# Kernel optimization log

Hardware: AMD Instinct MI355X
Metric: run time of the kernel (lower is better)

The kernel has to match this reference:

```python
import jax, jax.numpy as jnp
import numpy as np

OUT_SIZE = 14
CUTOFF = 0.2
VAR0 = 4            # var[0], mixin_factor = 0.0 -> current std = var[0]
BETA = 4.0
N_SQ = OUT_SIZE * OUT_SIZE
TAU = 0.5 / N_SQ
BATCH = 256
CHANNELS = 512


def _gkern_np(kernlen, std, vmin, vmax):
    n = np.arange(kernlen) - (kernlen - 1) / 2.0
    w = np.exp(-(n ** 2) / (2.0 * std * std))
    g = np.outer(w, w)
    return g * (vmax - vmin) + vmin


def _build_templates():
    n = OUT_SIZE
    base = _gkern_np(2 * n - 1, VAR0, -CUTOFF, 1.0)
    base = np.maximum(base, 0.0) * 2.0 - 1.0
    base = TAU * np.clip(BETA * base / n, -1.0, None)  # clamp(min=-1) only
    # unfold(0,n,1).unfold(1,n,1).reshape(-1,n,n) == sliding windows, row-major
    t = np.lib.stride_tricks.sliding_window_view(base, (n, n)).reshape(-1, n, n)
    t = np.flip(t, axis=0).copy()  # torch.flip(templates, dims=(0,))
    templates_f = jnp.asarray(t, jnp.float32)                    # (n^2, n, n)
    neg = -TAU * jnp.ones((1, n, n), jnp.float32)
    templates_b = jnp.concatenate([templates_f, neg], axis=0)    # (n^2+1, n, n)
    alpha = N_SQ / (1.0 + N_SQ)
    p_T = jnp.asarray(
        np.array([alpha / N_SQ] * N_SQ + [1.0 - alpha], np.float32))  # (n^2+1,)
    return templates_f, templates_b, p_T


def setup_inputs() -> dict:
    key = jax.random.key(0)
    templates_f, templates_b, p_T = _build_templates()
    x = jax.random.normal(key, (BATCH, CHANNELS, OUT_SIZE, OUT_SIZE), jnp.float32)
    return {"x": x, "templates_f": templates_f,
            "templates_b": templates_b, "p_T": p_T}


def reference(x, templates_f, templates_b, p_T):
    B, C, H, W = x.shape
    tau = 0.5 / (H * W)
    # max_pool2d with kernel == full spatial extent -> flat argmax per (b, c)
    idx = jnp.argmax(x.reshape(B, C, H * W), axis=-1)            # (B, C) int
    sel = templates_f[idx]                                       # (B, C, H, W)
    mask = sel / jnp.max(sel)                                    # global max
    mask = jax.nn.relu(mask - CUTOFF) / CUTOFF
    x_masked = x * mask
    # local loss (mutual-information style) on the masked activations
    tr_x_T = jnp.einsum('bcwh,twh->cbt', x_masked * tau, templates_b)  # (C,B,T)
    p_x_T = jax.nn.softmax(tr_x_T, axis=1)                       # softmax over b
    p_x = jnp.einsum('t,cbt->cb', p_T, p_x_T)                    # (C, B)
    log_ratio = jnp.log(p_x_T / p_x[:, :, None])                 # (C, B, T)
    p_x_T_log = jnp.einsum('cbt,cbt->ct', p_x_T, log_ratio)      # (C, T)
    loss = -jnp.einsum('t,ct->c', p_T, p_x_T_log)                # (C,)
    return x_masked, mask, loss
```

## Files before the change

kernel.cpp:

```cpp
#include <hip/hip_runtime.h>

#define BB 256
#define CCH 512
#define HW 196
#define TT 197
#define TROWS 208
#define NFRAG (13 * 7)
#define ASHORTS (NFRAG * 64 * 8)
#define H1FRAG (7 * 7)
#define H2FRAG (6 * 7)
#define H1SHORTS (H1FRAG * 512)
#define H2SHORTS (H2FRAG * 512)

typedef __attribute__((ext_vector_type(8))) short bf16x8;
typedef __attribute__((ext_vector_type(4))) float f32x4;

__device__ __forceinline__ unsigned short f2bf(float f) {
    union { float f; unsigned u; } v; v.f = f;
    unsigned r = v.u + 0x7FFFu + ((v.u >> 16) & 1u);
    return (unsigned short)(r >> 16);
}

__global__ void prep(const float* __restrict__ tf, const float* __restrict__ tb,
                     float* __restrict__ wsf, unsigned short* __restrict__ tb_bf) {
    if (blockIdx.x < 182) {
        int i = blockIdx.x * 256 + threadIdx.x;
        int frag = i >> 9;
        int s    = i & 511;
        int mt = frag / 7, kt = frag % 7;
        int lane = s >> 3, j = s & 7;
        int r = mt * 16 + (lane & 15);
        int k = kt * 32 + (lane >> 4) * 8 + j;
        const float tau = 0.5f / 196.0f;
        float v = (r < TT && k < HW) ? tb[r * HW + k] * tau : 0.0f;
        tb_bf[i] = f2bf(v);
    } else {
        __shared__ float red[256];
        float m = -1e30f;
        for (int i = threadIdx.x; i < HW * HW; i += 256) m = fmaxf(m, tf[i]);
        red[threadIdx.x] = m;
        __syncthreads();
        for (int s = 128; s > 0; s >>= 1) {
            if (threadIdx.x < s) red[threadIdx.x] = fmaxf(red[threadIdx.x], red[threadIdx.x + s]);
            __syncthreads();
        }
        if (threadIdx.x == 0) wsf[0] = red[0];
    }
}

extern "C" __global__ __launch_bounds__(1024)
void fused_one(const float* __restrict__ x, const float* __restrict__ tf,
               const float* __restrict__ pT, const unsigned short* __restrict__ tb_bf,
               const float* __restrict__ wsf,
               float* __restrict__ xm_out, float* __restrict__ mask_out,
               float* __restrict__ loss_out)
{
    extern __shared__ char smem[];
    unsigned short* Alds = (unsigned short*)smem;
    float* s_part = (float*)(smem + H1SHORTS * 2);
    float* rAs    = s_part + 16 * TROWS;
    float* lAs    = rAs + TROWS;
    float* pTs    = lAs + TROWS;
    float* red    = pTs + TROWS;

    const int c    = blockIdx.x;
    const int tid  = threadIdx.x;
    const int lane = tid & 63;
    const int w    = tid >> 6;
    const int l15  = lane & 15, lg = lane >> 4;
    const float rg = 1.0f / wsf[0];

    {
        const f32x4* src = (const f32x4*)tb_bf;
        f32x4* dst = (f32x4*)Alds;
        #pragma unroll
        for (int it = 0; it < 4; ++it) {
            int idx = tid + it * 1024;
            if (idx < H1SHORTS / 8) dst[idx] = src[idx];
        }
    }
    if (tid < TROWS) pTs[tid] = (tid < TT) ? pT[tid] : 0.0f;

    const int b = w * 16 + l15;
    const size_t rowoff = ((size_t)b * CCH + c) * HW;
    const float* xrow = x + rowoff;

    f32x4 u[13];
    #pragma unroll
    for (int kt = 0; kt < 6; ++kt) {
        u[2 * kt]     = *(const f32x4*)(xrow + kt * 32 + lg * 8);
        u[2 * kt + 1] = *(const f32x4*)(xrow + kt * 32 + lg * 8 + 4);
    }
    if (lg == 0) u[12] = *(const f32x4*)(xrow + 192);
    else         u[12] = (f32x4){-__builtin_inff(), -__builtin_inff(),
                                 -__builtin_inff(), -__builtin_inff()};

    float bv = -__builtin_inff(); int bi = 0;
    #pragma unroll
    for (int j = 0; j < 13; ++j) {
        const int k0 = (j < 12) ? (((j >> 1) * 8 + lg * 2 + (j & 1)) * 4) : 192;
        #pragma unroll
        for (int e = 0; e < 4; ++e) {
            float v = u[j][e];
            if (v > bv) { bv = v; bi = k0 + e; }
        }
    }
    #pragma unroll
    for (int m = 16; m <= 32; m <<= 1) {
        float ov = __shfl_xor(bv, m, 64);
        int   oi = __shfl_xor(bi, m, 64);
        if (ov > bv || (ov == bv && oi < bi)) { bv = ov; bi = oi; }
    }

    const float* selrow = tf + (size_t)bi * HW;
    float* xmrow = xm_out + rowoff;
    float* mkrow = mask_out + rowoff;
    bf16x8 fr[7];

    #pragma unroll
    for (int kt = 0; kt < 6; ++kt) {
        #pragma unroll
        for (int h = 0; h < 2; ++h) {
            const int k0 = kt * 32 + lg * 8 + h * 4;
            f32x4 sel = *(const f32x4*)(selrow + k0);
            f32x4 mk, xm;
            #pragma unroll
            for (int e = 0; e < 4; ++e) {
                float m = fmaxf(sel[e] * rg - 0.2f, 0.0f) * 5.0f;
                mk[e] = m;
                xm[e] = u[2 * kt + h][e] * m;
            }
            *(f32x4*)(xmrow + k0) = xm;
            *(f32x4*)(mkrow + k0) = mk;
            #pragma unroll
            for (int e = 0; e < 4; ++e) fr[kt][h * 4 + e] = (short)f2bf(xm[e]);
        }
    }
    {
        fr[6] = (bf16x8){0, 0, 0, 0, 0, 0, 0, 0};
        if (lg == 0) {
            f32x4 sel = *(const f32x4*)(selrow + 192);
            f32x4 mk, xm;
            #pragma unroll
            for (int e = 0; e < 4; ++e) {
                float m = fmaxf(sel[e] * rg - 0.2f, 0.0f) * 5.0f;
                mk[e] = m;
                xm[e] = u[12][e] * m;
            }
            *(f32x4*)(xmrow + 192) = xm;
            *(f32x4*)(mkrow + 192) = mk;
            #pragma unroll
            for (int e = 0; e < 4; ++e) fr[6][e] = (short)f2bf(xm[e]);
        }
    }

    __syncthreads();

    f32x4 acc[13];
    #pragma unroll
    for (int mt = 0; mt < 13; ++mt) acc[mt] = (f32x4){0.f, 0.f, 0.f, 0.f};

    const unsigned short* Abase = Alds + lane * 8;
    #pragma unroll
    for (int kt = 0; kt < 7; ++kt) {
        const bf16x8 bfrag = fr[kt];
        #pragma unroll
        for (int mt = 0; mt < 7; ++mt) {
            bf16x8 afrag = *(const bf16x8*)(Abase + (mt * 7 + kt) * 512);
            acc[mt] = __builtin_amdgcn_mfma_f32_16x16x32_bf16(afrag, bfrag, acc[mt], 0, 0, 0);
        }
    }

    __syncthreads();

    {
        const f32x4* src = (const f32x4*)(tb_bf + H1SHORTS);
        f32x4* dst = (f32x4*)Alds;
        #pragma unroll
        for (int it = 0; it < 3; ++it) {
            int idx = tid + it * 1024;
            if (idx < H2SHORTS / 8) dst[idx] = src[idx];
        }
    }
    __syncthreads();

    #pragma unroll
    for (int kt = 0; kt < 7; ++kt) {
        const bf16x8 bfrag = fr[kt];
        #pragma unroll
        for (int mt = 7; mt < 13; ++mt) {
            bf16x8 afrag = *(const bf16x8*)(Abase + ((mt - 7) * 7 + kt) * 512);
            acc[mt] = __builtin_amdgcn_mfma_f32_16x16x32_bf16(afrag, bfrag, acc[mt], 0, 0, 0);
        }
    }

    float* sp = s_part + w * TROWS;
    #pragma unroll
    for (int mt = 0; mt < 13; ++mt) {
        f32x4 s;
        #pragma unroll
        for (int e = 0; e < 4; ++e) s[e] = __expf(acc[mt][e]);
        #pragma unroll
        for (int m = 1; m <= 8; m <<= 1) {
            #pragma unroll
            for (int e = 0; e < 4; ++e) s[e] += __shfl_xor(s[e], m, 64);
        }
        if (l15 == 0) *(f32x4*)(sp + mt * 16 + lg * 4) = s;
    }
    __syncthreads();
    if (tid < TROWS) {
        float s = 0.f;
        #pragma unroll
        for (int w2 = 0; w2 < 16; ++w2) s += s_part[w2 * TROWS + tid];
        rAs[tid] = 1.0f / s;
        lAs[tid] = __logf(s);
    }
    __syncthreads();

    float px = 0.f;
    #pragma unroll
    for (int mt = 0; mt < 13; ++mt) {
        const int t0 = mt * 16 + lg * 4;
        f32x4 ra = *(const f32x4*)(rAs + t0);
        f32x4 pt = *(const f32x4*)(pTs + t0);
        #pragma unroll
        for (int e = 0; e < 4; ++e)
            px += pt[e] * __expf(acc[mt][e]) * ra[e];
    }
    px += __shfl_xor(px, 16, 64);
    px += __shfl_xor(px, 32, 64);
    const float lpx = __logf(px);

    float part = 0.f;
    #pragma unroll
    for (int mt = 0; mt < 13; ++mt) {
        const int t0 = mt * 16 + lg * 4;
        f32x4 ra = *(const f32x4*)(rAs + t0);
        f32x4 la = *(const f32x4*)(lAs + t0);
        f32x4 pt = *(const f32x4*)(pTs + t0);
        #pragma unroll
        for (int e = 0; e < 4; ++e) {
            float tr = acc[mt][e];
            float p  = __expf(tr) * ra[e];
            part += pt[e] * p * (tr - la[e] - lpx);
        }
    }
    #pragma unroll
    for (int off = 32; off >= 1; off >>= 1) part += __shfl_xor(part, off, 64);
    if (lane == 0) red[w] = part;
    __syncthreads();
    if (tid == 0) {
        float s = 0.f;
        #pragma unroll
        for (int w2 = 0; w2 < 16; ++w2) s += red[w2];
        loss_out[c] = -s;
    }
}

extern "C" void kernel_launch(void* const* d_in, const int* in_sizes, int n_in,
                              void* d_out, int out_size, void* d_ws, size_t ws_size,
                              hipStream_t stream) {
    const float* x  = (const float*)d_in[0];
    const float* tf = (const float*)d_in[1];
    const float* tb = (const float*)d_in[2];
    const float* pT = (const float*)d_in[3];

    const size_t NOUT = (size_t)BB * CCH * HW;
    float* xm_out = (float*)d_out;
    float* mk_out = xm_out + NOUT;
    float* ls_out = mk_out + NOUT;

    float* wsf = (float*)d_ws;
    unsigned short* tb_bf = (unsigned short*)((char*)d_ws + 64);

    prep<<<183, 256, 0, stream>>>(tf, tb, wsf, tb_bf);

    const size_t SMEM = (size_t)H1SHORTS * 2
                      + 16 * TROWS * 4
                      + 3 * TROWS * 4 + 16 * 4;
    (void)hipFuncSetAttribute((const void*)fused_one,
                              hipFuncAttributeMaxDynamicSharedMemorySize, (int)SMEM);
    fused_one<<<dim3(CCH), dim3(1024), SMEM, stream>>>(x, tf, pT, tb_bf, wsf,
                                                       xm_out, mk_out, ls_out);
}
```

Before: 168.6 us.

## Recompute MFMA scores in a second pass to cut register pressure

The kernel no longer keeps 13 accumulator tiles and 13 x vectors live in registers. It computes each score tile, reduces its exp sums, and discards it, then reloads both template halves into LDS and redoes the MFMAs for the loss pass. The loss is rewritten algebraically as S1 - px*log(px), so a single pass accumulates both terms, and __launch_bounds__ now asks for higher occupancy. The price is twice the MFMA work, extra LDS reloads and barriers, and x being read from global memory twice.

```diff
diff --git a/kernel.cpp b/kernel.cpp
--- a/kernel.cpp
+++ b/kernel.cpp
@@ -5,8 +5,6 @@
 #define HW 196
 #define TT 197
 #define TROWS 208
-#define NFRAG (13 * 7)
-#define ASHORTS (NFRAG * 64 * 8)
 #define H1FRAG (7 * 7)
 #define H2FRAG (6 * 7)
 #define H1SHORTS (H1FRAG * 512)
@@ -48,7 +46,7 @@
     }
 }
 
-extern "C" __global__ __launch_bounds__(1024)
+extern "C" __global__ __launch_bounds__(1024, 8)
 void fused_one(const float* __restrict__ x, const float* __restrict__ tf,
                const float* __restrict__ pT, const unsigned short* __restrict__ tb_bf,
                const float* __restrict__ wsf,
@@ -85,24 +83,17 @@
     const size_t rowoff = ((size_t)b * CCH + c) * HW;
     const float* xrow = x + rowoff;
 
-    f32x4 u[13];
-    #pragma unroll
-    for (int kt = 0; kt < 6; ++kt) {
-        u[2 * kt]     = *(const f32x4*)(xrow + kt * 32 + lg * 8);
-        u[2 * kt + 1] = *(const f32x4*)(xrow + kt * 32 + lg * 8 + 4);
-    }
-    if (lg == 0) u[12] = *(const f32x4*)(xrow + 192);
-    else         u[12] = (f32x4){-__builtin_inff(), -__builtin_inff(),
-                                 -__builtin_inff(), -__builtin_inff()};
-
     float bv = -__builtin_inff(); int bi = 0;
     #pragma unroll
     for (int j = 0; j < 13; ++j) {
-        const int k0 = (j < 12) ? (((j >> 1) * 8 + lg * 2 + (j & 1)) * 4) : 192;
-        #pragma unroll
-        for (int e = 0; e < 4; ++e) {
-            float v = u[j][e];
-            if (v > bv) { bv = v; bi = k0 + e; }
+        const int k0 = (j < 12) ? ((j >> 1) * 32 + lg * 8 + (j & 1) * 4) : 192;
+        if (j < 12 || lg == 0) {
+            f32x4 xv = *(const f32x4*)(xrow + k0);
+            #pragma unroll
+            for (int e = 0; e < 4; ++e) {
+                float v = xv[e];
+                if (v > bv) { bv = v; bi = k0 + e; }
+            }
         }
     }
     #pragma unroll
@@ -123,12 +114,13 @@
         for (int h = 0; h < 2; ++h) {
             const int k0 = kt * 32 + lg * 8 + h * 4;
             f32x4 sel = *(const f32x4*)(selrow + k0);
+            f32x4 xv  = *(const f32x4*)(xrow + k0);
             f32x4 mk, xm;
             #pragma unroll
             for (int e = 0; e < 4; ++e) {
                 float m = fmaxf(sel[e] * rg - 0.2f, 0.0f) * 5.0f;
                 mk[e] = m;
-                xm[e] = u[2 * kt + h][e] * m;
+                xm[e] = xv[e] * m;
             }
             *(f32x4*)(xmrow + k0) = xm;
             *(f32x4*)(mkrow + k0) = mk;
@@ -140,12 +132,13 @@
         fr[6] = (bf16x8){0, 0, 0, 0, 0, 0, 0, 0};
         if (lg == 0) {
             f32x4 sel = *(const f32x4*)(selrow + 192);
+            f32x4 xv  = *(const f32x4*)(xrow + 192);
             f32x4 mk, xm;
             #pragma unroll
             for (int e = 0; e < 4; ++e) {
                 float m = fmaxf(sel[e] * rg - 0.2f, 0.0f) * 5.0f;
                 mk[e] = m;
-                xm[e] = u[12][e] * m;
+                xm[e] = xv[e] * m;
             }
             *(f32x4*)(xmrow + 192) = xm;
             *(f32x4*)(mkrow + 192) = mk;
@@ -156,23 +149,28 @@
 
     __syncthreads();
 
-    f32x4 acc[13];
-    #pragma unroll
-    for (int mt = 0; mt < 13; ++mt) acc[mt] = (f32x4){0.f, 0.f, 0.f, 0.f};
-
     const unsigned short* Abase = Alds + lane * 8;
-    #pragma unroll
-    for (int kt = 0; kt < 7; ++kt) {
-        const bf16x8 bfrag = fr[kt];
-        #pragma unroll
-        for (int mt = 0; mt < 7; ++mt) {
-            bf16x8 afrag = *(const bf16x8*)(Abase + (mt * 7 + kt) * 512);
-            acc[mt] = __builtin_amdgcn_mfma_f32_16x16x32_bf16(afrag, bfrag, acc[mt], 0, 0, 0);
-        }
-    }
-
-    __syncthreads();
-
+    float* sp = s_part + w * TROWS;
+
+    #pragma unroll
+    for (int mt = 0; mt < 7; ++mt) {
+        f32x4 acc = (f32x4){0.f, 0.f, 0.f, 0.f};
+        #pragma unroll
+        for (int kt = 0; kt < 7; ++kt)
+            acc = __builtin_amdgcn_mfma_f32_16x16x32_bf16(
+                *(const bf16x8*)(Abase + (mt * 7 + kt) * 512), fr[kt], acc, 0, 0, 0);
+        f32x4 s;
+        #pragma unroll
+        for (int e = 0; e < 4; ++e) s[e] = __expf(acc[e]);
+        #pragma unroll
+        for (int m = 1; m <= 8; m <<= 1) {
+            #pragma unroll
+            for (int e = 0; e < 4; ++e) s[e] += __shfl_xor(s[e], m, 64);
+        }
+        if (l15 == 0) *(f32x4*)(sp + mt * 16 + lg * 4) = s;
+    }
+
+    __syncthreads();
     {
         const f32x4* src = (const f32x4*)(tb_bf + H1SHORTS);
         f32x4* dst = (f32x4*)Alds;
@@ -185,21 +183,15 @@
     __syncthreads();
 
     #pragma unroll
-    for (int kt = 0; kt < 7; ++kt) {
-        const bf16x8 bfrag = fr[kt];
-        #pragma unroll
-        for (int mt = 7; mt < 13; ++mt) {
-            bf16x8 afrag = *(const bf16x8*)(Abase + ((mt - 7) * 7 + kt) * 512);
-            acc[mt] = __builtin_amdgcn_mfma_f32_16x16x32_bf16(afrag, bfrag, acc[mt], 0, 0, 0);
-        }
-    }
-
-    float* sp = s_part + w * TROWS;
-    #pragma unroll
-    for (int mt = 0; mt < 13; ++mt) {
+    for (int mt = 7; mt < 13; ++mt) {
+        f32x4 acc = (f32x4){0.f, 0.f, 0.f, 0.f};
+        #pragma unroll
+        for (int kt = 0; kt < 7; ++kt)
+            acc = __builtin_amdgcn_mfma_f32_16x16x32_bf16(
+                *(const bf16x8*)(Abase + ((mt - 7) * 7 + kt) * 512), fr[kt], acc, 0, 0, 0);
         f32x4 s;
         #pragma unroll
-        for (int e = 0; e < 4; ++e) s[e] = __expf(acc[mt][e]);
+        for (int e = 0; e < 4; ++e) s[e] = __expf(acc[e]);
         #pragma unroll
         for (int m = 1; m <= 8; m <<= 1) {
             #pragma unroll
@@ -207,7 +199,9 @@
         }
         if (l15 == 0) *(f32x4*)(sp + mt * 16 + lg * 4) = s;
     }
-    __syncthreads();
+
+    __syncthreads();
+
     if (tid < TROWS) {
         float s = 0.f;
         #pragma unroll
@@ -215,38 +209,75 @@
         rAs[tid] = 1.0f / s;
         lAs[tid] = __logf(s);
     }
-    __syncthreads();
-
-    float px = 0.f;
-    #pragma unroll
-    for (int mt = 0; mt < 13; ++mt) {
-        const int t0 = mt * 16 + lg * 4;
-        f32x4 ra = *(const f32x4*)(rAs + t0);
-        f32x4 pt = *(const f32x4*)(pTs + t0);
-        #pragma unroll
-        for (int e = 0; e < 4; ++e)
-            px += pt[e] * __expf(acc[mt][e]) * ra[e];
-    }
-    px += __shfl_xor(px, 16, 64);
-    px += __shfl_xor(px, 32, 64);
-    const float lpx = __logf(px);
-
-    float part = 0.f;
-    #pragma unroll
-    for (int mt = 0; mt < 13; ++mt) {
+    {
+        const f32x4* src = (const f32x4*)tb_bf;
+        f32x4* dst = (f32x4*)Alds;
+        #pragma unroll
+        for (int it = 0; it < 4; ++it) {
+            int idx = tid + it * 1024;
+            if (idx < H1SHORTS / 8) dst[idx] = src[idx];
+        }
+    }
+    __syncthreads();
+
+    float px = 0.f, S1 = 0.f;
+    #pragma unroll
+    for (int mt = 0; mt < 7; ++mt) {
+        f32x4 acc = (f32x4){0.f, 0.f, 0.f, 0.f};
+        #pragma unroll
+        for (int kt = 0; kt < 7; ++kt)
+            acc = __builtin_amdgcn_mfma_f32_16x16x32_bf16(
+                *(const bf16x8*)(Abase + (mt * 7 + kt) * 512), fr[kt], acc, 0, 0, 0);
         const int t0 = mt * 16 + lg * 4;
         f32x4 ra = *(const f32x4*)(rAs + t0);
         f32x4 la = *(const f32x4*)(lAs + t0);
         f32x4 pt = *(const f32x4*)(pTs + t0);
         #pragma unroll
         for (int e = 0; e < 4; ++e) {
-            float tr = acc[mt][e];
-            float p  = __expf(tr) * ra[e];
-            part += pt[e] * p * (tr - la[e] - lpx);
-        }
-    }
-    #pragma unroll
-    for (int off = 32; off >= 1; off >>= 1) part += __shfl_xor(part, off, 64);
+            float p = __expf(acc[e]) * ra[e];
+            px += pt[e] * p;
+            S1 += pt[e] * p * (acc[e] - la[e]);
+        }
+    }
+
+    __syncthreads();
+    {
+        const f32x4* src = (const f32x4*)(tb_bf + H1SHORTS);
+        f32x4* dst = (f32x4*)Alds;
+        #pragma unroll
+        for (int it = 0; it < 3; ++it) {
+            int idx = tid + it * 1024;
+            if (idx < H2SHORTS / 8) dst[idx] = src[idx];
+        }
+    }
+    __syncthreads();
+
+    #pragma unroll
+    for (int mt = 7; mt < 13; ++mt) {
+        f32x4 acc = (f32x4){0.f, 0.f, 0.f, 0.f};
+        #pragma unroll
+        for (int kt = 0; kt < 7; ++kt)
+            acc = __builtin_amdgcn_mfma_f32_16x16x32_bf16(
+                *(const bf16x8*)(Abase + ((mt - 7) * 7 + kt) * 512), fr[kt], acc, 0, 0, 0);
+        const int t0 = mt * 16 + lg * 4;
+        f32x4 ra = *(const f32x4*)(rAs + t0);
+        f32x4 la = *(const f32x4*)(lAs + t0);
+        f32x4 pt = *(const f32x4*)(pTs + t0);
+        #pragma unroll
+        for (int e = 0; e < 4; ++e) {
+            float p = __expf(acc[e]) * ra[e];
+            px += pt[e] * p;
+            S1 += pt[e] * p * (acc[e] - la[e]);
+        }
+    }
+
+    px += __shfl_xor(px, 16, 64);
+    px += __shfl_xor(px, 32, 64);
+    S1 += __shfl_xor(S1, 16, 64);
+    S1 += __shfl_xor(S1, 32, 64);
+    float part = S1 - px * __logf(px);
+    #pragma unroll
+    for (int m = 1; m <= 8; m <<= 1) part += __shfl_xor(part, m, 64);
     if (lane == 0) red[w] = part;
     __syncthreads();
     if (tid == 0) {
```

Measured after the change: 388.1 us. 130% more time.
